# Kernel tuning notes

Measured on AMD Instinct MI355X. Metric: run time of the kernel, lower is better.

The kernel has to match this reference:

```python
import jax, jax.numpy as jnp
import numpy as np

N = 50000
E = 600000
D = 128


def gcn_conv(x, row, col, w, W, b):
    """PyG GCNConv: add self-loops (weight 1), symmetric deg^-1/2 normalization,
    linear transform, edge-weighted scatter-add aggregation, then bias."""
    n = x.shape[0]
    loop = jnp.arange(n)
    r = jnp.concatenate([row, loop])            # source nodes, [E+N]
    c = jnp.concatenate([col, loop])            # target nodes, [E+N]
    ww = jnp.concatenate([w, jnp.ones((n,), x.dtype)])
    deg = jax.ops.segment_sum(ww, c, num_segments=n)          # weighted in-degree
    dinv = jnp.where(deg > 0, jax.lax.rsqrt(deg), jnp.zeros_like(deg))
    norm = dinv[r] * ww * dinv[c]               # [E+N]
    xl = x @ W                                  # [n, D_out]
    msg = norm[:, None] * xl[r]                 # gather + scale, [E+N, D_out]
    out = jax.ops.segment_sum(msg, c, num_segments=n)
    return out + b


def setup_inputs() -> dict:
    key = jax.random.key(0)
    ks = jax.random.split(key, 12)
    x = jax.random.normal(ks[0], (N, D), dtype=jnp.float32)
    edge_index = jax.random.randint(ks[1], (2, E), 0, N, dtype=jnp.int64)
    edge_weights = jax.random.uniform(ks[2], (E,), dtype=jnp.float32)
    s = 1.0 / np.sqrt(D)
    W1 = jax.random.uniform(ks[3], (D, D), jnp.float32, -s, s)
    b1 = jnp.zeros((D,), jnp.float32)
    W2 = jax.random.uniform(ks[4], (D, D), jnp.float32, -s, s)
    b2 = jnp.zeros((D,), jnp.float32)
    W3 = jax.random.uniform(ks[5], (D, D), jnp.float32, -s, s)
    b3 = jnp.zeros((D,), jnp.float32)
    prelu_w = jnp.array(0.25, jnp.float32)
    return {"x": x, "edge_index": edge_index, "edge_weights": edge_weights,
            "W1": W1, "b1": b1, "W2": W2, "b2": b2, "W3": W3, "b3": b3,
            "prelu_w": prelu_w}


def reference(x, edge_index, edge_weights, W1, b1, W2, b2, W3, b3, prelu_w):
    row, col = edge_index[0], edge_index[1]
    # layer 1: GCNConv -> (dropout: eval, identity) -> ELU
    h = gcn_conv(x, row, col, edge_weights, W1, b1)
    h = jax.nn.elu(h)
    # layer 2: GCNConv -> GELU (torch default = exact erf)
    h = gcn_conv(h, row, col, edge_weights, W2, b2)
    h = jax.nn.gelu(h, approximate=False)
    # layer 3: GCNConv -> PReLU (learnable scalar slope)
    h = gcn_conv(h, row, col, edge_weights, W3, b3)
    h = jnp.where(h >= 0, h, prelu_w * h)
    return h
```

## Files before the change

kernel.cpp:

```cpp
#include <hip/hip_runtime.h>
#include <hip/hip_fp16.h>
#include <math.h>
#include <string.h>

constexpr int D = 128;

struct __align__(16) H8 { __half2 h[4]; };
struct __align__(8)  H4 { __half2 a, b; };

typedef _Float16 half8  __attribute__((ext_vector_type(8)));
typedef float   floatx4 __attribute__((ext_vector_type(4)));
typedef int     i32x4   __attribute__((ext_vector_type(4)));

template <typename T>
__device__ __forceinline__ T ld_nt(const T* p) {
  i32x4 v = __builtin_nontemporal_load((const i32x4*)p);
  T r; memcpy(&r, &v, 16); return r;
}
__device__ __forceinline__ void st_nt8(void* p, float2 v) {
  long long t; memcpy(&t, &v, 8);
  __builtin_nontemporal_store(t, (long long*)p);
}


__device__ __forceinline__ int detect64(const int* __restrict__ ei) {
  int z = 0;
#pragma unroll
  for (int i = 0; i < 8; ++i) z |= ei[2 * i + 1];
  return (z == 0) ? 1 : 0;
}

__device__ __forceinline__ void load_edge(const int* __restrict__ ei, int e, int nE,
                                          int m64, int n, int& r, int& c) {
  if (m64) { r = ei[2 * (size_t)e]; c = ei[2 * ((size_t)nE + e)]; }
  else     { r = ei[(size_t)e];     c = ei[(size_t)nE + e]; }
  r = min(max(r, 0), n - 1);
  c = min(max(c, 0), n - 1);
}

__global__ void k_init(const float* __restrict__ W1, const float* __restrict__ W2,
                       const float* __restrict__ W3, __half* __restrict__ Wt,
                       int* __restrict__ cnt, int n) {
  __shared__ float s[128][129];
  int tid = threadIdx.x;
  if (blockIdx.x >= 3) {
    int i = (blockIdx.x - 3) * 256 + tid;
    if (i < n) cnt[i] = 0;
    return;
  }
  const float* W = blockIdx.x == 0 ? W1 : (blockIdx.x == 1 ? W2 : W3);
  __half* o = Wt + (size_t)blockIdx.x * D * D;
#pragma unroll
  for (int i = 0; i < 16; ++i) {
    int flat = i * 1024 + tid * 4;
    int k = flat >> 7;
    int nn = flat & 127;
    float4 v = *(const float4*)(W + (size_t)k * D + nn);
    s[k][nn] = v.x; s[k][nn + 1] = v.y; s[k][nn + 2] = v.z; s[k][nn + 3] = v.w;
  }
  __syncthreads();
#pragma unroll
  for (int i = 0; i < 8; ++i) {
    int flat = i * 256 + tid;
    int nn = flat >> 4;
    int k0 = (flat & 15) * 8;
    H8 hv;
#pragma unroll
    for (int t = 0; t < 4; ++t)
      hv.h[t] = __floats2half2_rn(s[k0 + 2 * t][nn], s[k0 + 2 * t + 1][nn]);
    *(H8*)(o + (size_t)nn * D + k0) = hv;
  }
}

__global__ void k_pos(const int* __restrict__ ei, int* __restrict__ cnt,
                      unsigned int* __restrict__ rcp, int* __restrict__ pos,
                      int nE, int n) {
  int e = blockIdx.x * blockDim.x + threadIdx.x;
  if (e >= nE) return;
  int m64 = detect64(ei);
  int r, c;
  load_edge(ei, e, nE, m64, n, r, c);
  rcp[e] = ((unsigned int)r << 16) | (unsigned int)c;
  pos[e] = atomicAdd(&cnt[c], 1);
}

__global__ __launch_bounds__(1024) void k_scan(const int* __restrict__ cnt,
                                               int* __restrict__ offs, int n, int nE) {
  __shared__ int wsx[16];
  __shared__ int tot;
  const int t = threadIdx.x;
  const int lane = t & 63, wid = t >> 6;
  int carry = 0;
  for (int base = 0; base < n; base += 1024) {
    int i = base + t;
    int v = (i < n) ? cnt[i] : 0;
    int s = v;
#pragma unroll
    for (int d = 1; d < 64; d <<= 1) {
      int x = __shfl_up(s, d, 64);
      if (lane >= d) s += x;
    }
    if (lane == 63) wsx[wid] = s;
    __syncthreads();
    if (t < 16) {
      int ws = wsx[t];
      int ss = ws;
#pragma unroll
      for (int d = 1; d < 16; d <<= 1) {
        int x = __shfl_up(ss, d, 16);
        if (t >= d) ss += x;
      }
      wsx[t] = ss - ws;
      if (t == 15) tot = ss;
    }
    __syncthreads();
    if (i < n) offs[i] = carry + wsx[wid] + (s - v);
    carry += tot;
    __syncthreads();
  }
  if (t == 0) offs[n] = nE;
}

__global__ void k_fill(const unsigned int* __restrict__ rcp, const int* __restrict__ pos,
                       const float* __restrict__ w, const int* __restrict__ offs,
                       unsigned int* __restrict__ ecf2, int nE) {
  int e = blockIdx.x * blockDim.x + threadIdx.x;
  if (e >= nE) return;
  unsigned int p = rcp[e];
  int idx = offs[p & 0xffffu] + pos[e];
  ecf2[idx] = (p & 0xffff0000u) |
              (unsigned int)__half_as_ushort(__float2half_rn(w[e]));
}

__global__ void k_degdinv(const unsigned int* __restrict__ ecf2, const int* __restrict__ offs,
                          float* __restrict__ dinv, int n) {
  int i = blockIdx.x * blockDim.x + threadIdx.x;
  if (i >= n) return;
  float s = 1.0f;
  int e1 = offs[i + 1];
  for (int e = offs[i]; e < e1; ++e)
    s += __half2float(__ushort_as_half((unsigned short)(ecf2[e] & 0xffffu)));
  dinv[i] = rsqrtf(s);
}

template <int ACT>
__device__ __forceinline__ float act_f(float x) {
  if (ACT == 1) return x > 0.f ? x : expm1f(x);
  if (ACT == 2) return 0.5f * x * (1.0f + erff(x * 0.70710678118654752440f));
  return x;
}

template <int ACT, typename AT>
__global__ __launch_bounds__(256) void k_gemm(const AT* __restrict__ A,
                                              const __half* __restrict__ Wt,
                                              const float* __restrict__ dinv,
                                              __half* __restrict__ Z, int n) {
  const int wave = threadIdx.x >> 6;
  const int lane = threadIdx.x & 63;
  const int np = lane & 15;
  const int quad = lane >> 4;
  const int node = blockIdx.x * 64 + wave * 16 + np;
  const int nc = min(node, n - 1);

  half8 b[4];
#pragma unroll
  for (int s = 0; s < 4; ++s) {
    if constexpr (sizeof(AT) == 4) {
      const float* ap = (const float*)A + (size_t)nc * D + s * 32 + quad * 8;
      float4 v0 = ld_nt((const float4*)ap);
      float4 v1 = ld_nt((const float4*)(ap + 4));
      b[s][0] = (_Float16)act_f<ACT>(v0.x); b[s][1] = (_Float16)act_f<ACT>(v0.y);
      b[s][2] = (_Float16)act_f<ACT>(v0.z); b[s][3] = (_Float16)act_f<ACT>(v0.w);
      b[s][4] = (_Float16)act_f<ACT>(v1.x); b[s][5] = (_Float16)act_f<ACT>(v1.y);
      b[s][6] = (_Float16)act_f<ACT>(v1.z); b[s][7] = (_Float16)act_f<ACT>(v1.w);
    } else {
      half8 raw = *(const half8*)((const __half*)A + ((size_t)s * n + nc) * 32 + quad * 8);
#pragma unroll
      for (int t = 0; t < 8; ++t)
        b[s][t] = (_Float16)act_f<ACT>((float)raw[t]);
    }
  }

  floatx4 acc[8];
#pragma unroll
  for (int mt = 0; mt < 8; ++mt) acc[mt] = (floatx4){0.f, 0.f, 0.f, 0.f};

#pragma unroll
  for (int mt = 0; mt < 8; ++mt) {
#pragma unroll
    for (int s = 0; s < 4; ++s) {
      half8 a = *(const half8*)(Wt + (size_t)(mt * 16 + np) * D + s * 32 + quad * 8);
      acc[mt] = __builtin_amdgcn_mfma_f32_16x16x32_f16(a, b[s], acc[mt], 0, 0, 0);
    }
  }

  if (node < n) {
    float dv = dinv[node];
#pragma unroll
    for (int mt = 0; mt < 8; ++mt) {
      H4 hv;
      hv.a = __floats2half2_rn(dv * acc[mt][0], dv * acc[mt][1]);
      hv.b = __floats2half2_rn(dv * acc[mt][2], dv * acc[mt][3]);
      int f0 = mt * 16 + quad * 4;
      *(H4*)(Z + ((size_t)(f0 >> 5) * n + node) * 32 + (f0 & 31)) = hv;
    }
  }
}

__device__ __forceinline__ void fmacc8(float* acc, float c, const H8& y) {
  float2 f;
  f = __half22float2(y.h[0]); acc[0] += c * f.x; acc[1] += c * f.y;
  f = __half22float2(y.h[1]); acc[2] += c * f.x; acc[3] += c * f.y;
  f = __half22float2(y.h[2]); acc[4] += c * f.x; acc[5] += c * f.y;
  f = __half22float2(y.h[3]); acc[6] += c * f.x; acc[7] += c * f.y;
}

__device__ __forceinline__ float cdecode(unsigned int u) {
  return __half2float(__ushort_as_half((unsigned short)(u & 0xffffu)));
}

template <int PRELU, typename OutT>
__global__ __launch_bounds__(256) void k_agg(const __half* __restrict__ Z,
                                             const int* __restrict__ offs,
                                             const unsigned int* __restrict__ ecf2,
                                             const float* __restrict__ dinv,
                                             const float* __restrict__ bias,
                                             const float* __restrict__ pw,
                                             OutT* __restrict__ OUT, int n) {
  const int chunk = blockIdx.x & 3;
  const int t = threadIdx.x;
  const int node = (blockIdx.x >> 2) * 16 + (t >> 4);
  const int sub = (t >> 2) & 3;
  const int j = t & 3;
  if (node >= n) return;
  const __half* Zc = Z + (size_t)chunk * n * 32;
  float acc[8] = {0.f, 0.f, 0.f, 0.f, 0.f, 0.f, 0.f, 0.f};
  if (sub == 0) {
    H8 zs = *(const H8*)(Zc + (size_t)node * 32 + j * 8);
    fmacc8(acc, 1.0f, zs);
  }
  int e0 = offs[node], e1 = offs[node + 1];
  int e = e0 + sub;
  for (; e + 12 < e1; e += 16) {
    unsigned int u0 = ecf2[e],     u1 = ecf2[e + 4];
    unsigned int u2 = ecf2[e + 8], u3 = ecf2[e + 12];
    H8 z0 = *(const H8*)(Zc + (size_t)(u0 >> 16) * 32 + j * 8);
    H8 z1 = *(const H8*)(Zc + (size_t)(u1 >> 16) * 32 + j * 8);
    H8 z2 = *(const H8*)(Zc + (size_t)(u2 >> 16) * 32 + j * 8);
    H8 z3 = *(const H8*)(Zc + (size_t)(u3 >> 16) * 32 + j * 8);
    fmacc8(acc, cdecode(u0), z0);
    fmacc8(acc, cdecode(u1), z1);
    fmacc8(acc, cdecode(u2), z2);
    fmacc8(acc, cdecode(u3), z3);
  }
  for (; e + 4 < e1; e += 8) {
    unsigned int u0 = ecf2[e], u1 = ecf2[e + 4];
    H8 z0 = *(const H8*)(Zc + (size_t)(u0 >> 16) * 32 + j * 8);
    H8 z1 = *(const H8*)(Zc + (size_t)(u1 >> 16) * 32 + j * 8);
    fmacc8(acc, cdecode(u0), z0);
    fmacc8(acc, cdecode(u1), z1);
  }
  for (; e < e1; e += 4) {
    unsigned int u = ecf2[e];
    H8 z = *(const H8*)(Zc + (size_t)(u >> 16) * 32 + j * 8);
    fmacc8(acc, cdecode(u), z);
  }
#pragma unroll
  for (int i = 0; i < 8; ++i) {
    acc[i] += __shfl_xor(acc[i], 4, 64);
    acc[i] += __shfl_xor(acc[i], 8, 64);
  }
  float dc = dinv[node];
  const float* bp = bias + chunk * 32 + j * 8 + sub * 2;
  float o0 = dc * acc[sub * 2 + 0] + bp[0];
  float o1 = dc * acc[sub * 2 + 1] + bp[1];
  if (PRELU) {
    float wv = *pw;
    o0 = o0 >= 0.f ? o0 : wv * o0;
    o1 = o1 >= 0.f ? o1 : wv * o1;
  }
  if constexpr (sizeof(OutT) == 4) {
    st_nt8((float*)OUT + (size_t)node * D + chunk * 32 + j * 8 + sub * 2,
           make_float2(o0, o1));
  } else {
    *(__half2*)((__half*)OUT + ((size_t)chunk * n + node) * 32 + j * 8 + sub * 2) =
        __floats2half2_rn(o0, o1);
  }
}

extern "C" void kernel_launch(void* const* d_in, const int* in_sizes, int n_in,
                              void* d_out, int out_size, void* d_ws, size_t ws_size,
                              hipStream_t stream) {
  const float* x  = (const float*)d_in[0];
  const int*   ei = (const int*)d_in[1];
  const float* w  = (const float*)d_in[2];
  const float* W1 = (const float*)d_in[3];
  const float* b1 = (const float*)d_in[4];
  const float* W2 = (const float*)d_in[5];
  const float* b2 = (const float*)d_in[6];
  const float* W3 = (const float*)d_in[7];
  const float* b3 = (const float*)d_in[8];
  const float* pw = (const float*)d_in[9];
  const int N = in_sizes[0] / D;
  const int E = in_sizes[2];
  float* out = (float*)d_out;

  char* wsb = (char*)d_ws;
  size_t off = 0;
  auto alloc = [&](size_t bytes) {
    void* p = wsb + off;
    off = (off + bytes + 255) & ~(size_t)255;
    return p;
  };
  float*        dinv = (float*)alloc((size_t)N * 4);
  int*          cnt  = (int*)alloc((size_t)N * 4);
  int*          offs = (int*)alloc((size_t)(N + 1) * 4);
  unsigned int* ecf2 = (unsigned int*)alloc((size_t)E * 4);
  __half*       Wt   = (__half*)alloc((size_t)3 * D * D * 2);
  __half*       Z    = (__half*)alloc((size_t)N * D * 2);
  __half*       h    = (__half*)alloc((size_t)N * D * 2);
  unsigned int* rcp  = (unsigned int*)Z;
  int*          pos  = (int*)((char*)Z + (size_t)E * 4);

  const int nb = (N + 255) / 256;
  const int eb = (E + 255) / 256;

  hipLaunchKernelGGL(k_init,    dim3(3 + nb), dim3(256), 0, stream, W1, W2, W3, Wt, cnt, N);
  hipLaunchKernelGGL(k_pos,     dim3(eb), dim3(256), 0, stream, ei, cnt, rcp, pos, E, N);
  hipLaunchKernelGGL(k_scan,    dim3(1),  dim3(1024), 0, stream, cnt, offs, N, E);
  hipLaunchKernelGGL(k_fill,    dim3(eb), dim3(256), 0, stream, rcp, pos, w, offs, ecf2, E);
  hipLaunchKernelGGL(k_degdinv, dim3(nb), dim3(256), 0, stream, ecf2, offs, dinv, N);

  const int gb = (N + 63) / 64;
  const int ab = 4 * ((N + 15) / 16);

  hipLaunchKernelGGL((k_gemm<0, float>),  dim3(gb), dim3(256), 0, stream, x, Wt,             dinv, Z, N);
  hipLaunchKernelGGL((k_agg<0, __half>),  dim3(ab), dim3(256), 0, stream, Z, offs, ecf2, dinv, b1, pw, h, N);
  hipLaunchKernelGGL((k_gemm<1, __half>), dim3(gb), dim3(256), 0, stream, h, Wt + D * D,     dinv, Z, N);
  hipLaunchKernelGGL((k_agg<0, __half>),  dim3(ab), dim3(256), 0, stream, Z, offs, ecf2, dinv, b2, pw, h, N);
  hipLaunchKernelGGL((k_gemm<2, __half>), dim3(gb), dim3(256), 0, stream, h, Wt + 2 * D * D, dinv, Z, N);
  hipLaunchKernelGGL((k_agg<1, float>),   dim3(ab), dim3(256), 0, stream, Z, offs, ecf2, dinv, b3, pw, out, N);
}
```

Baseline: 344.2 us.

## Replace single-block prefix scan with three-phase multi-block scan

Swaps the single 1024-thread block that scanned all node counts serially in chunks for a three-kernel scan: per-block local scans, a scan of the block sums, then an add-back pass. This is meant to spread the scan across many CUs instead of one block looping about 49 times. It adds two extra kernel launches, and k_scan2 only handles up to 256 blocks, which limits N to 65536.

```diff
diff --git a/kernel.cpp b/kernel.cpp
--- a/kernel.cpp
+++ b/kernel.cpp
@@ -84,41 +84,45 @@
   pos[e] = atomicAdd(&cnt[c], 1);
 }
 
-__global__ __launch_bounds__(1024) void k_scan(const int* __restrict__ cnt,
-                                               int* __restrict__ offs, int n, int nE) {
-  __shared__ int wsx[16];
-  __shared__ int tot;
-  const int t = threadIdx.x;
-  const int lane = t & 63, wid = t >> 6;
-  int carry = 0;
-  for (int base = 0; base < n; base += 1024) {
-    int i = base + t;
-    int v = (i < n) ? cnt[i] : 0;
-    int s = v;
-#pragma unroll
-    for (int d = 1; d < 64; d <<= 1) {
-      int x = __shfl_up(s, d, 64);
-      if (lane >= d) s += x;
-    }
-    if (lane == 63) wsx[wid] = s;
+__global__ void k_scan1(const int* __restrict__ cnt, int* __restrict__ offs,
+                        int* __restrict__ bsum, int n) {
+  __shared__ int s[256];
+  int t = threadIdx.x;
+  int i = blockIdx.x * 256 + t;
+  int v = (i < n) ? cnt[i] : 0;
+  s[t] = v;
+  __syncthreads();
+  for (int off = 1; off < 256; off <<= 1) {
+    int x = 0;
+    if (t >= off) x = s[t - off];
     __syncthreads();
-    if (t < 16) {
-      int ws = wsx[t];
-      int ss = ws;
-#pragma unroll
-      for (int d = 1; d < 16; d <<= 1) {
-        int x = __shfl_up(ss, d, 16);
-        if (t >= d) ss += x;
-      }
-      wsx[t] = ss - ws;
-      if (t == 15) tot = ss;
-    }
+    if (t >= off) s[t] += x;
     __syncthreads();
-    if (i < n) offs[i] = carry + wsx[wid] + (s - v);
-    carry += tot;
+  }
+  if (i < n) offs[i] = s[t] - v;
+  if (t == 255) bsum[blockIdx.x] = s[255];
+}
+
+__global__ void k_scan2(const int* __restrict__ bsum, int* __restrict__ boff, int nb) {
+  __shared__ int s[256];
+  int t = threadIdx.x;
+  int v = (t < nb) ? bsum[t] : 0;
+  s[t] = v;
+  __syncthreads();
+  for (int off = 1; off < 256; off <<= 1) {
+    int x = 0;
+    if (t >= off) x = s[t - off];
     __syncthreads();
-  }
-  if (t == 0) offs[n] = nE;
+    if (t >= off) s[t] += x;
+    __syncthreads();
+  }
+  if (t < nb) boff[t] = s[t] - v;
+}
+
+__global__ void k_scan3(int* __restrict__ offs, const int* __restrict__ boff, int n, int nE) {
+  int i = blockIdx.x * 256 + threadIdx.x;
+  if (i < n) offs[i] += boff[blockIdx.x];
+  if (i == 0) offs[n] = nE;
 }
 
 __global__ void k_fill(const unsigned int* __restrict__ rcp, const int* __restrict__ pos,
@@ -315,6 +319,8 @@
   float*        dinv = (float*)alloc((size_t)N * 4);
   int*          cnt  = (int*)alloc((size_t)N * 4);
   int*          offs = (int*)alloc((size_t)(N + 1) * 4);
+  int*          bsum = (int*)alloc(256 * 4);
+  int*          boff = (int*)alloc(256 * 4);
   unsigned int* ecf2 = (unsigned int*)alloc((size_t)E * 4);
   __half*       Wt   = (__half*)alloc((size_t)3 * D * D * 2);
   __half*       Z    = (__half*)alloc((size_t)N * D * 2);
@@ -327,7 +333,9 @@
 
   hipLaunchKernelGGL(k_init,    dim3(3 + nb), dim3(256), 0, stream, W1, W2, W3, Wt, cnt, N);
   hipLaunchKernelGGL(k_pos,     dim3(eb), dim3(256), 0, stream, ei, cnt, rcp, pos, E, N);
-  hipLaunchKernelGGL(k_scan,    dim3(1),  dim3(1024), 0, stream, cnt, offs, N, E);
+  hipLaunchKernelGGL(k_scan1,   dim3(nb), dim3(256), 0, stream, cnt, offs, bsum, N);
+  hipLaunchKernelGGL(k_scan2,   dim3(1),  dim3(256), 0, stream, bsum, boff, nb);
+  hipLaunchKernelGGL(k_scan3,   dim3(nb), dim3(256), 0, stream, offs, boff, N, E);
   hipLaunchKernelGGL(k_fill,    dim3(eb), dim3(256), 0, stream, rcp, pos, w, offs, ecf2, E);
   hipLaunchKernelGGL(k_degdinv, dim3(nb), dim3(256), 0, stream, ecf2, offs, dinv, N);
 
```

Result: faster. 305.8 us (-11.2%).
